# Kernel optimization log

Hardware: AMD Instinct MI355X
Metric: run time of the kernel (lower is better)

The kernel has to match this reference:

```python
import jax, jax.numpy as jnp
import numpy as np

HIDDEN = 768
MLP = 4 * HIDDEN

def layernorm(x, g, b, eps=1e-5):
    mu = jnp.mean(x, axis=-1, keepdims=True)
    var = jnp.var(x, axis=-1, keepdims=True)
    return (x - mu) * jax.lax.rsqrt(var + eps) * g + b

def setup_inputs() -> dict:
    key = jax.random.key(0)
    ks = jax.random.split(key, 10)
    b, l, h = 8, 1024, HIDDEN
    s = 1.0 / np.sqrt(h)
    inp = {
        "x": jax.random.normal(ks[0], (b, l, h), dtype=jnp.float32),
        "Wq": jax.random.normal(ks[1], (h, h), dtype=jnp.float32) * s,
        "Wk": jax.random.normal(ks[2], (h, h), dtype=jnp.float32) * s,
        "Wv": jax.random.normal(ks[3], (h, h), dtype=jnp.float32) * s,
        "Wo": jax.random.normal(ks[4], (h, h), dtype=jnp.float32) * s,
        "W1": jax.random.normal(ks[5], (h, MLP), dtype=jnp.float32) * s,
        "b1": jnp.zeros((MLP,), dtype=jnp.float32),
        "W2": jax.random.normal(ks[6], (MLP, h), dtype=jnp.float32) * (1.0 / np.sqrt(MLP)),
        "b2": jnp.zeros((h,), dtype=jnp.float32),
        "g1": jnp.ones((h,), dtype=jnp.float32),
        "be1": jnp.zeros((h,), dtype=jnp.float32),
        "g2": jnp.ones((h,), dtype=jnp.float32),
        "be2": jnp.zeros((h,), dtype=jnp.float32),
        "n_heads": 12,
    }
    return inp

def reference(x, Wq, Wk, Wv, Wo, W1, b1, W2, b2, g1, be1, g2, be2, n_heads):
    b, l, h = x.shape
    d = h // n_heads
    # NOTE: faithful to source — heads are the LAST axis of a plain reshape,
    # and the second einsum contracts with K (not V), reproducing the original code.
    q = (x @ Wq).reshape(b, l, d, n_heads)
    k = (x @ Wk).reshape(b, l, d, n_heads)
    v = (x @ Wv).reshape(b, l, d, n_heads)  # computed but unused downstream, as in source
    scores = jnp.einsum('bldn,bmdn->blmn', q, k) / (d ** 0.5)
    attn = jax.nn.softmax(scores, axis=2)  # softmax over m (dim=2), as in source
    ctx = jnp.einsum('blmn,bmdn->bldn', attn, k).reshape(b, l, h)
    attn_out = ctx @ Wo
    x = x + attn_out
    x = layernorm(x, g1, be1)
    ff = (jax.nn.gelu(x @ W1 + b1, approximate=False) @ W2) + b2
    x = x + ff
    x = layernorm(x, g2, be2)
    return x
```

## Files before the change

### kernel.cpp

```cpp
#include <hip/hip_runtime.h>
#include <math.h>

typedef unsigned short u16;
typedef unsigned int u32;
typedef short bf16x8 __attribute__((ext_vector_type(8)));
typedef float f32x4 __attribute__((ext_vector_type(4)));

#define MFMA(a, b, c) __builtin_amdgcn_mfma_f32_16x16x32_bf16((a), (b), (c), 0, 0, 0)

#define GLOAD_LDS16(g, l)                                                              \
    __builtin_amdgcn_global_load_lds((const __attribute__((address_space(1))) void*)(g), \
                                     (__attribute__((address_space(3))) void*)(l), 16, 0, 0)

__device__ __forceinline__ u16 f2bf(float f) {
    u32 u = __float_as_uint(f);
    u32 r = (u + 0x7fffu + ((u >> 16) & 1u)) >> 16;
    return (u16)r;
}

__device__ __forceinline__ float fast_gelu(float z) {
    float u = fminf(1.5957691216f * z * (1.0f + 0.044715f * z * z), 80.0f);
    float e = __expf(u);
    float r = __builtin_amdgcn_rcpf(e + 1.0f);
    return z * e * r;
}

__global__ __launch_bounds__(256) void f32_to_bf16_k(const float* __restrict__ in,
                                                     u16* __restrict__ out) {
    size_t i = ((size_t)blockIdx.x * 256 + threadIdx.x) * 8;
    const float4* p = reinterpret_cast<const float4*>(in + i);
    float4 a = p[0], b = p[1];
    union { u16 u[8]; uint4 v; } o;
    o.u[0] = f2bf(a.x); o.u[1] = f2bf(a.y); o.u[2] = f2bf(a.z); o.u[3] = f2bf(a.w);
    o.u[4] = f2bf(b.x); o.u[5] = f2bf(b.y); o.u[6] = f2bf(b.z); o.u[7] = f2bf(b.w);
    *reinterpret_cast<uint4*>(out + i) = o.v;
}

__global__ __launch_bounds__(256) void transpose_bf16_k(const float* __restrict__ in,
                                                        u16* __restrict__ out,
                                                        int K, int N) {
    __shared__ float tile[64][65];
    int k0 = blockIdx.y * 64, n0 = blockIdx.x * 64;
    int t = threadIdx.x;
    for (int p = 0; p < 16; p++) {
        int idx = t + p * 256;
        int r = idx >> 6, c = idx & 63;
        tile[r][c] = in[(size_t)(k0 + r) * N + n0 + c];
    }
    __syncthreads();
    for (int p = 0; p < 16; p++) {
        int idx = t + p * 256;
        int nr = idx >> 6, nc = idx & 63;
        out[(size_t)(n0 + nr) * K + k0 + nc] = f2bf(tile[nc][nr]);
    }
}

__global__ __launch_bounds__(256) void transpose_wo_k(const float* __restrict__ in,
                                                      u16* __restrict__ out) {
    __shared__ float tile[96][65];
    int k0 = blockIdx.y * 96, n0 = blockIdx.x * 64;
    int t = threadIdx.x;
    for (int p = 0; p < 24; p++) {
        int idx = t + p * 256;
        int r = idx >> 6, c = idx & 63;
        tile[r][c] = in[(size_t)(k0 + r) * 768 + n0 + c];
    }
    __syncthreads();
    for (int p = 0; p < 3; p++) {
        int idx = t + p * 256;
        int c = idx / 12, n = idx % 12;
        union { u16 u[8]; uint4 v; } o;
        for (int j = 0; j < 8; j++) o.u[j] = f2bf(tile[j * 12 + n][c]);
        *reinterpret_cast<uint4*>(&out[(size_t)(n0 + c) * 768 + n * 64 + blockIdx.y * 8]) = o.v;
    }
}

__global__ __launch_bounds__(256) void head_pack_k(const u16* __restrict__ in, int ld,
                                                   u16* __restrict__ out) {
    __shared__ u16 tile[16 * 768];
    int b = blockIdx.y;
    int l0 = blockIdx.x * 16;
    int t = threadIdx.x;
    for (int p = 0; p < 6; p++) {
        int c = t + p * 256;
        int li = c / 96, dc = c % 96;
        *reinterpret_cast<uint4*>(&tile[li * 768 + dc * 8]) =
            *reinterpret_cast<const uint4*>(&in[(size_t)(b * 1024 + l0 + li) * ld + dc * 8]);
    }
    __syncthreads();
    for (int p = 0; p < 6; p++) {
        int c = t + p * 256;
        int n = c >> 7, rem = c & 127, li = rem >> 3, k8 = rem & 7;
        union { u16 u[8]; uint4 v; } o;
        for (int j = 0; j < 8; j++) o.u[j] = tile[li * 768 + (k8 * 8 + j) * 12 + n];
        *reinterpret_cast<uint4*>(&out[(size_t)((b * 12 + n) * 1024 + l0 + li) * 64 + k8 * 8]) = o.v;
    }
}

template <int EPI, int TM, bool AH = false>
__global__ __launch_bounds__(256) void gemm_bt_k(const u16* __restrict__ A,
                                                 const u16* __restrict__ BT,
                                                 int M, int N, int K, int NBX,
                                                 float* __restrict__ outF,
                                                 u16* __restrict__ outB,
                                                 const float* __restrict__ resid,
                                                 const float* __restrict__ bias) {
    constexpr int MI = TM / 32;
    constexpr int NS = (TM == 64) ? 4 : 3;
    __shared__ __align__(16) u16 As[NS][TM * 32];
    __shared__ __align__(16) u16 Bs[NS][128 * 32];

    int L = blockIdx.x;
    int bx = (L >> 3) % NBX;
    int by = (L / (8 * NBX)) * 8 + (L & 7);
    int m0 = by * TM, n0 = bx * 128;

    int t = threadIdx.x;
    int wave = t >> 6, lane = t & 63;
    int wr = (wave >> 1) * (TM / 2), wc = (wave & 1) * 64;
    int ln = lane & 15, quad = lane >> 4;
    int sw = quad ^ ((ln >> 1) & 3);

    int e0 = t, e1 = t + 256;
    int r0 = e0 >> 2, c0 = (e0 & 3) ^ ((r0 >> 1) & 3);
    int r1 = e1 >> 2, c1 = (e1 & 3) ^ ((r1 >> 1) & 3);
    const u16* A0 = A + (size_t)(m0 + r0) * K + c0 * 8;
    const u16* A1 = A + (size_t)(m0 + r1) * K + c1 * 8;
    const u16* B0 = BT + (size_t)(n0 + r0) * K + c0 * 8;
    const u16* B1 = BT + (size_t)(n0 + r1) * K + c1 * 8;
    const u16* Abase = nullptr;
    if constexpr (AH) {
        int m = m0 + r0;
        Abase = A + ((size_t)(m >> 10) * 12288 + (m & 1023)) * 64;
    }

    int nk = K >> 5;

    f32x4 acc[MI][4];
    for (int i = 0; i < MI; i++)
        for (int j = 0; j < 4; j++)
            for (int r = 0; r < 4; r++) acc[i][j][r] = 0.0f;

    for (int s = 0; s < NS - 1; s++) {
        if constexpr (AH) {
            int col8 = s * 4 + c0;
            GLOAD_LDS16(Abase + (col8 >> 3) * 65536 + (col8 & 7) * 8, &As[s][e0 * 8]);
        } else {
            GLOAD_LDS16(A0 + s * 32, &As[s][e0 * 8]);
            if constexpr (TM == 128) GLOAD_LDS16(A1 + s * 32, &As[s][e1 * 8]);
        }
        GLOAD_LDS16(B0 + s * 32, &Bs[s][e0 * 8]);
        GLOAD_LDS16(B1 + s * 32, &Bs[s][e1 * 8]);
    }

    for (int k = 0; k < nk; k++) {
        if constexpr (TM == 64) asm volatile("s_waitcnt vmcnt(6)" ::: "memory");
        else                    asm volatile("s_waitcnt vmcnt(4)" ::: "memory");
        asm volatile("s_barrier" ::: "memory");
        {
            int ks = k + NS - 1 < nk ? k + NS - 1 : nk - 1;
            int bi = (k + NS - 1) % NS;
            if constexpr (AH) {
                int col8 = ks * 4 + c0;
                GLOAD_LDS16(Abase + (col8 >> 3) * 65536 + (col8 & 7) * 8, &As[bi][e0 * 8]);
            } else {
                GLOAD_LDS16(A0 + ks * 32, &As[bi][e0 * 8]);
                if constexpr (TM == 128) GLOAD_LDS16(A1 + ks * 32, &As[bi][e1 * 8]);
            }
            GLOAD_LDS16(B0 + ks * 32, &Bs[bi][e0 * 8]);
            GLOAD_LDS16(B1 + ks * 32, &Bs[bi][e1 * 8]);
        }
        const u16* as = As[k % NS];
        const u16* bs = Bs[k % NS];
        bf16x8 afr[MI], bfr[4];
        for (int i = 0; i < MI; i++)
            afr[i] = *reinterpret_cast<const bf16x8*>(&as[(wr + i * 16 + ln) * 32 + sw * 8]);
        for (int j = 0; j < 4; j++)
            bfr[j] = *reinterpret_cast<const bf16x8*>(&bs[(wc + j * 16 + ln) * 32 + sw * 8]);
        for (int i = 0; i < MI; i++)
            for (int j = 0; j < 4; j++)
                acc[i][j] = MFMA(afr[i], bfr[j], acc[i][j]);
    }

    for (int i = 0; i < MI; i++) {
        for (int j = 0; j < 4; j++) {
            int col = n0 + wc + j * 16 + ln;
            for (int r = 0; r < 4; r++) {
                int row = m0 + wr + i * 16 + quad * 4 + r;
                size_t idx = (size_t)row * N + col;
                float v = acc[i][j][r];
                if constexpr (EPI == 0) {
                    outB[idx] = f2bf(v);
                } else if constexpr (EPI == 1) {
                    outF[idx] = resid[idx] + v;
                } else if constexpr (EPI == 2) {
                    outB[idx] = f2bf(fast_gelu(v + bias[col]));
                } else if constexpr (EPI == 3) {
                    outF[idx] = resid[idx] + v + bias[col];
                } else {
                    outB[idx] = f2bf(col < 768 ? v * 0.125f : v);
                }
            }
        }
    }
}

__global__ __launch_bounds__(256) void attention_k(const u16* __restrict__ QB, int ldq,
                                                   const u16* __restrict__ KH,
                                                   u16* __restrict__ CTXH) {
    __shared__ __align__(16) u16 Ks[64 * 72];
    __shared__ __align__(16) u16 KsT[64 * 72];
    __shared__ __align__(16) u16 Pl[4][16 * 64];
    int bh = blockIdx.y;
    int b = bh / 12, n = bh % 12;
    int l0 = blockIdx.x * 64;
    int t = threadIdx.x, wave = t >> 6, lane = t & 63;
    int ln = lane & 15, quad = lane >> 4;
    int lw = l0 + wave * 16;

    bf16x8 a0, a1;
    {
        union { u16 u[8]; bf16x8 v; } q0, q1;
        const u16* qrow = QB + (size_t)(b * 1024 + lw + ln) * ldq + n;
        for (int j = 0; j < 8; j++) {
            q0.u[j] = qrow[(quad * 8 + j) * 12];
            q1.u[j] = qrow[(32 + quad * 8 + j) * 12];
        }
        a0 = q0.v; a1 = q1.v;
    }

    f32x4 o[4];
    for (int dt = 0; dt < 4; dt++)
        for (int r = 0; r < 4; r++) o[dt][r] = 0.0f;
    float lst[4];
    for (int r = 0; r < 4; r++) lst[r] = 0.0f;

    const u16* Kbase = KH + (size_t)bh * 1024 * 64;
    int mi = t & 63, ds = (t >> 6) * 16;
    int psw = (ln >> 2) & 3;

    union { u16 u[8]; uint4 v; } kva, kvb;
    kva.v = *reinterpret_cast<const uint4*>(&Kbase[(size_t)mi * 64 + ds]);
    kvb.v = *reinterpret_cast<const uint4*>(&Kbase[(size_t)mi * 64 + ds + 8]);

    for (int mb = 0; mb < 16; mb++) {
        __syncthreads();
        *reinterpret_cast<uint4*>(&Ks[mi * 72 + ds]) = kva.v;
        *reinterpret_cast<uint4*>(&Ks[mi * 72 + ds + 8]) = kvb.v;
        for (int j = 0; j < 8; j++) KsT[(ds + j) * 72 + mi] = kva.u[j];
        for (int j = 0; j < 8; j++) KsT[(ds + 8 + j) * 72 + mi] = kvb.u[j];
        __syncthreads();

        {
            int mnext = (mb + 1 < 16 ? mb + 1 : 15) * 64;
            kva.v = *reinterpret_cast<const uint4*>(&Kbase[(size_t)(mnext + mi) * 64 + ds]);
            kvb.v = *reinterpret_cast<const uint4*>(&Kbase[(size_t)(mnext + mi) * 64 + ds + 8]);
        }

        f32x4 st[4];
        for (int nt = 0; nt < 4; nt++) {
            bf16x8 bk0 = *reinterpret_cast<bf16x8*>(&Ks[(nt * 16 + ln) * 72 + quad * 8]);
            bf16x8 bk1 = *reinterpret_cast<bf16x8*>(&Ks[(nt * 16 + ln) * 72 + 32 + quad * 8]);
            f32x4 z;
            for (int r = 0; r < 4; r++) z[r] = 0.0f;
            z = MFMA(a0, bk0, z);
            st[nt] = MFMA(a1, bk1, z);
        }

        for (int r = 0; r < 4; r++) {
            int row = quad * 4 + r;
            float psum = 0.0f;
            for (int nt = 0; nt < 4; nt++) {
                float p = __expf(fminf(st[nt][r], 30.0f));
                psum += p;
                Pl[wave][row * 64 + (((nt * 2 + (ln >> 3)) ^ quad) * 8) + (ln & 7)] = f2bf(p);
            }
            lst[r] += psum;
        }

        bf16x8 pf0 = *reinterpret_cast<bf16x8*>(&Pl[wave][ln * 64 + (quad ^ psw) * 8]);
        bf16x8 pf1 = *reinterpret_cast<bf16x8*>(&Pl[wave][ln * 64 + (quad ^ psw) * 8 + 32]);
        for (int dt = 0; dt < 4; dt++) {
            bf16x8 bk0 = *reinterpret_cast<bf16x8*>(&KsT[(dt * 16 + ln) * 72 + quad * 8]);
            bf16x8 bk1 = *reinterpret_cast<bf16x8*>(&KsT[(dt * 16 + ln) * 72 + 32 + quad * 8]);
            o[dt] = MFMA(pf0, bk0, o[dt]);
            o[dt] = MFMA(pf1, bk1, o[dt]);
        }
    }

    for (int r = 0; r < 4; r++)
        for (int off = 1; off < 16; off <<= 1) lst[r] += __shfl_xor(lst[r], off, 64);

    u16* out = CTXH + (size_t)bh * 1024 * 64;
    for (int r = 0; r < 4; r++) {
        float inv = 1.0f / lst[r];
        int row = lw + quad * 4 + r;
        for (int dt = 0; dt < 4; dt++)
            out[(size_t)row * 64 + dt * 16 + ln] = f2bf(o[dt][r] * inv);
    }
}

__global__ __launch_bounds__(256) void layernorm_k(const float* __restrict__ in,
                                                   float* __restrict__ outF,
                                                   u16* __restrict__ outB,
                                                   const float* __restrict__ g,
                                                   const float* __restrict__ be) {
    __shared__ float red[8];
    int row = blockIdx.x;
    int t = threadIdx.x;
    const float* p = in + (size_t)row * 768;
    float v0 = p[t], v1 = p[t + 256], v2 = p[t + 512];
    float s = v0 + v1 + v2;
    float ss = v0 * v0 + v1 * v1 + v2 * v2;
    for (int off = 32; off >= 1; off >>= 1) {
        s += __shfl_xor(s, off, 64);
        ss += __shfl_xor(ss, off, 64);
    }
    int wave = t >> 6, lane = t & 63;
    if (lane == 0) { red[wave] = s; red[4 + wave] = ss; }
    __syncthreads();
    float S = red[0] + red[1] + red[2] + red[3];
    float SS = red[4] + red[5] + red[6] + red[7];
    float mean = S * (1.0f / 768.0f);
    float var = SS * (1.0f / 768.0f) - mean * mean;
    float rstd = rsqrtf(var + 1e-5f);
    float o0 = (v0 - mean) * rstd * g[t] + be[t];
    float o1 = (v1 - mean) * rstd * g[t + 256] + be[t + 256];
    float o2 = (v2 - mean) * rstd * g[t + 512] + be[t + 512];
    float* q = outF + (size_t)row * 768;
    q[t] = o0; q[t + 256] = o1; q[t + 512] = o2;
    if (outB) {
        u16* qb = outB + (size_t)row * 768;
        qb[t] = f2bf(o0); qb[t + 256] = f2bf(o1); qb[t + 512] = f2bf(o2);
    }
}

extern "C" void kernel_launch(void* const* d_in, const int* in_sizes, int n_in,
                              void* d_out, int out_size, void* d_ws, size_t ws_size,
                              hipStream_t stream) {
    const float* x   = (const float*)d_in[0];
    const float* Wq  = (const float*)d_in[1];
    const float* Wk  = (const float*)d_in[2];
    const float* Wo  = (const float*)d_in[4];
    const float* W1  = (const float*)d_in[5];
    const float* b1  = (const float*)d_in[6];
    const float* W2  = (const float*)d_in[7];
    const float* b2  = (const float*)d_in[8];
    const float* g1  = (const float*)d_in[9];
    const float* be1 = (const float*)d_in[10];
    const float* g2  = (const float*)d_in[11];
    const float* be2 = (const float*)d_in[12];
    float* out = (float*)d_out;

    const int S = 8192, H = 768, MLP4 = 3072, H2 = 1536;

    char* ws = (char*)d_ws;
    u16* XB   = (u16*)ws;  ws += (size_t)S * H * 2;
    u16* WQKT = (u16*)ws;  ws += (size_t)H2 * H * 2;
    u16* WOT  = (u16*)ws;  ws += (size_t)H * H * 2;
    u16* W1T  = (u16*)ws;  ws += (size_t)H * MLP4 * 2;
    u16* W2T  = (u16*)ws;  ws += (size_t)H * MLP4 * 2;
    u16* QKB  = (u16*)ws;  ws += (size_t)S * H2 * 2;
    u16* KH   = (u16*)ws;  ws += (size_t)S * H * 2;
    float* Y  = (float*)ws; ws += (size_t)S * H * 4;
    u16* HB   = (u16*)ws;  ws += (size_t)S * MLP4 * 2;

    u16* CTXH = XB;
    u16* X1B  = QKB;

    f32_to_bf16_k<<<(S * H) / 2048, 256, 0, stream>>>(x, XB);
    transpose_bf16_k<<<dim3(12, 12), 256, 0, stream>>>(Wq, WQKT, H, H);
    transpose_bf16_k<<<dim3(12, 12), 256, 0, stream>>>(Wk, WQKT + (size_t)H * H, H, H);
    transpose_wo_k<<<dim3(12, 8), 256, 0, stream>>>(Wo, WOT);
    transpose_bf16_k<<<dim3(48, 12), 256, 0, stream>>>(W1, W1T, H, MLP4);
    transpose_bf16_k<<<dim3(12, 48), 256, 0, stream>>>(W2, W2T, MLP4, H);

    gemm_bt_k<4, 128><<<12 * 64, 256, 0, stream>>>(XB, WQKT, S, H2, H, 12, nullptr, QKB, nullptr, nullptr);

    head_pack_k<<<dim3(64, 8), 256, 0, stream>>>(QKB + H, H2, KH);
    attention_k<<<dim3(16, 96), 256, 0, stream>>>(QKB, H2, KH, CTXH);

    gemm_bt_k<1, 64, true><<<6 * 128, 256, 0, stream>>>(CTXH, WOT, S, H, H, 6, Y, nullptr, x, nullptr);
    layernorm_k<<<S, 256, 0, stream>>>(Y, Y, X1B, g1, be1);

    gemm_bt_k<2, 128><<<24 * 64, 256, 0, stream>>>(X1B, W1T, S, MLP4, H, 24, nullptr, HB, nullptr, b1);
    gemm_bt_k<3, 64><<<6 * 128, 256, 0, stream>>>(HB, W2T, S, H, MLP4, 6, Y, nullptr, Y, b2);
    layernorm_k<<<S, 256, 0, stream>>>(Y, out, nullptr, g2, be2);
}
```

Measured before the change: 412.4 us.

## Merge weight prep into one kernel and use 128x256 tiles for wide GEMMs

Replaces the six separate cast and transpose launches with a single prep kernel that dispatches on block index. Adds a larger-tile GEMM (128x256, 4x8 MFMA fragments per wave, 3-stage pipeline, launch bounds min 2 blocks) for the QK projection and the W1+GELU GEMM, which raises arithmetic intensity per LDS load. The costs are many more accumulator registers per thread and fewer blocks, so occupancy and wave balance may suffer. The smaller GEMMs stay on the 64-row tile kernel.

```diff
diff --git a/kernel.cpp b/kernel.cpp
--- a/kernel.cpp
+++ b/kernel.cpp
@@ -25,9 +25,8 @@
     return z * e * r;
 }
 
-__global__ __launch_bounds__(256) void f32_to_bf16_k(const float* __restrict__ in,
-                                                     u16* __restrict__ out) {
-    size_t i = ((size_t)blockIdx.x * 256 + threadIdx.x) * 8;
+__device__ void dev_xcast(const float* __restrict__ in, u16* __restrict__ out, int blk) {
+    size_t i = ((size_t)blk * 256 + threadIdx.x) * 8;
     const float4* p = reinterpret_cast<const float4*>(in + i);
     float4 a = p[0], b = p[1];
     union { u16 u[8]; uint4 v; } o;
@@ -36,42 +35,67 @@
     *reinterpret_cast<uint4*>(out + i) = o.v;
 }
 
-__global__ __launch_bounds__(256) void transpose_bf16_k(const float* __restrict__ in,
-                                                        u16* __restrict__ out,
-                                                        int K, int N) {
-    __shared__ float tile[64][65];
-    int k0 = blockIdx.y * 64, n0 = blockIdx.x * 64;
+__device__ void dev_transpose(const float* __restrict__ in, u16* __restrict__ out,
+                              int K, int N, int bx, int by, float* tile ) {
+    int k0 = by * 64, n0 = bx * 64;
     int t = threadIdx.x;
     for (int p = 0; p < 16; p++) {
         int idx = t + p * 256;
         int r = idx >> 6, c = idx & 63;
-        tile[r][c] = in[(size_t)(k0 + r) * N + n0 + c];
+        tile[r * 65 + c] = in[(size_t)(k0 + r) * N + n0 + c];
     }
     __syncthreads();
     for (int p = 0; p < 16; p++) {
         int idx = t + p * 256;
         int nr = idx >> 6, nc = idx & 63;
-        out[(size_t)(n0 + nr) * K + k0 + nc] = f2bf(tile[nc][nr]);
-    }
-}
-
-__global__ __launch_bounds__(256) void transpose_wo_k(const float* __restrict__ in,
-                                                      u16* __restrict__ out) {
-    __shared__ float tile[96][65];
-    int k0 = blockIdx.y * 96, n0 = blockIdx.x * 64;
+        out[(size_t)(n0 + nr) * K + k0 + nc] = f2bf(tile[nc * 65 + nr]);
+    }
+}
+
+__device__ void dev_wo(const float* __restrict__ in, u16* __restrict__ out,
+                       int bx, int by, float* tile ) {
+    int k0 = by * 96, n0 = bx * 64;
     int t = threadIdx.x;
     for (int p = 0; p < 24; p++) {
         int idx = t + p * 256;
         int r = idx >> 6, c = idx & 63;
-        tile[r][c] = in[(size_t)(k0 + r) * 768 + n0 + c];
+        tile[r * 65 + c] = in[(size_t)(k0 + r) * 768 + n0 + c];
     }
     __syncthreads();
     for (int p = 0; p < 3; p++) {
         int idx = t + p * 256;
         int c = idx / 12, n = idx % 12;
         union { u16 u[8]; uint4 v; } o;
-        for (int j = 0; j < 8; j++) o.u[j] = f2bf(tile[j * 12 + n][c]);
-        *reinterpret_cast<uint4*>(&out[(size_t)(n0 + c) * 768 + n * 64 + blockIdx.y * 8]) = o.v;
+        for (int j = 0; j < 8; j++) o.u[j] = f2bf(tile[(j * 12 + n) * 65 + c]);
+        *reinterpret_cast<uint4*>(&out[(size_t)(n0 + c) * 768 + n * 64 + by * 8]) = o.v;
+    }
+}
+
+__global__ __launch_bounds__(256) void prep_k(const float* __restrict__ x,
+                                              const float* __restrict__ Wq,
+                                              const float* __restrict__ Wk,
+                                              const float* __restrict__ Wo,
+                                              const float* __restrict__ W1,
+                                              const float* __restrict__ W2,
+                                              u16* __restrict__ XB,
+                                              u16* __restrict__ WQKT,
+                                              u16* __restrict__ WOT,
+                                              u16* __restrict__ W1T,
+                                              u16* __restrict__ W2T) {
+    __shared__ float tile[96 * 65];
+    int bid = blockIdx.x;
+    if (bid < 3072) {
+        dev_xcast(x, XB, bid);
+    } else if (bid < 3216) {
+        int b = bid - 3072; dev_transpose(Wq, WQKT, 768, 768, b % 12, b / 12, tile);
+    } else if (bid < 3360) {
+        int b = bid - 3216; dev_transpose(Wk, WQKT + (size_t)768 * 768, 768, 768, b % 12, b / 12, tile);
+    } else if (bid < 3456) {
+        int b = bid - 3360; dev_wo(Wo, WOT, b % 12, b / 12, tile);
+    } else if (bid < 4032) {
+        int b = bid - 3456; dev_transpose(W1, W1T, 768, 3072, b % 48, b / 48, tile);
+    } else {
+        int b = bid - 4032; dev_transpose(W2, W2T, 3072, 768, b % 12, b / 12, tile);
     }
 }
 
@@ -97,27 +121,107 @@
     }
 }
 
-template <int EPI, int TM, bool AH = false>
+template <int EPI>
+__global__ __launch_bounds__(256, 2) void gemm_big_k(const u16* __restrict__ A,
+                                                     const u16* __restrict__ BT,
+                                                     int M, int N, int K, int NBX,
+                                                     u16* __restrict__ outB,
+                                                     const float* __restrict__ bias) {
+    __shared__ __align__(16) u16 As[3][128 * 32];
+    __shared__ __align__(16) u16 Bs[3][256 * 32];
+    int L = blockIdx.x;
+    int bx = (L >> 3) % NBX;
+    int by = (L / (8 * NBX)) * 8 + (L & 7);
+    int m0 = by * 128, n0 = bx * 256;
+    int t = threadIdx.x, wave = t >> 6, lane = t & 63;
+    int wr = (wave >> 1) * 64, wc = (wave & 1) * 128;
+    int ln = lane & 15, quad = lane >> 4;
+    int sw = quad ^ ((ln >> 1) & 3);
+
+    int ra0 = t >> 2,          ca0 = (t & 3) ^ ((ra0 >> 1) & 3);
+    int ra1 = (t + 256) >> 2,  ca1 = (t & 3) ^ ((ra1 >> 1) & 3);
+    const u16* Ap0 = A + (size_t)(m0 + ra0) * K + ca0 * 8;
+    const u16* Ap1 = A + (size_t)(m0 + ra1) * K + ca1 * 8;
+    const u16* Bp[4];
+    int eoff[4];
+    for (int g = 0; g < 4; g++) {
+        int e = t + 256 * g;
+        int r = e >> 2, c = (e & 3) ^ ((r >> 1) & 3);
+        Bp[g] = BT + (size_t)(n0 + r) * K + c * 8;
+        eoff[g] = e * 8;
+    }
+
+    int nk = K >> 5;
+
+    f32x4 acc[4][8];
+    for (int i = 0; i < 4; i++)
+        for (int j = 0; j < 8; j++)
+            for (int r = 0; r < 4; r++) acc[i][j][r] = 0.0f;
+
+    for (int s = 0; s < 2; s++) {
+        GLOAD_LDS16(Ap0 + s * 32, &As[s][t * 8]);
+        GLOAD_LDS16(Ap1 + s * 32, &As[s][(t + 256) * 8]);
+        for (int g = 0; g < 4; g++) GLOAD_LDS16(Bp[g] + s * 32, &Bs[s][eoff[g]]);
+    }
+
+    for (int k = 0; k < nk; k++) {
+        asm volatile("s_waitcnt vmcnt(6)" ::: "memory");
+        asm volatile("s_barrier" ::: "memory");
+        {
+            int ks = k + 2 < nk ? k + 2 : nk - 1;
+            int bi = (k + 2) % 3;
+            GLOAD_LDS16(Ap0 + ks * 32, &As[bi][t * 8]);
+            GLOAD_LDS16(Ap1 + ks * 32, &As[bi][(t + 256) * 8]);
+            for (int g = 0; g < 4; g++) GLOAD_LDS16(Bp[g] + ks * 32, &Bs[bi][eoff[g]]);
+        }
+        const u16* as = As[k % 3];
+        const u16* bs = Bs[k % 3];
+        bf16x8 afr[4], bfr[8];
+        for (int i = 0; i < 4; i++)
+            afr[i] = *reinterpret_cast<const bf16x8*>(&as[(wr + i * 16 + ln) * 32 + sw * 8]);
+        for (int j = 0; j < 8; j++)
+            bfr[j] = *reinterpret_cast<const bf16x8*>(&bs[(wc + j * 16 + ln) * 32 + sw * 8]);
+        for (int i = 0; i < 4; i++)
+            for (int j = 0; j < 8; j++)
+                acc[i][j] = MFMA(afr[i], bfr[j], acc[i][j]);
+    }
+
+    for (int i = 0; i < 4; i++) {
+        for (int j = 0; j < 8; j++) {
+            int col = n0 + wc + j * 16 + ln;
+            for (int r = 0; r < 4; r++) {
+                int row = m0 + wr + i * 16 + quad * 4 + r;
+                size_t idx = (size_t)row * N + col;
+                float v = acc[i][j][r];
+                if constexpr (EPI == 2) {
+                    outB[idx] = f2bf(fast_gelu(v + bias[col]));
+                } else {
+                    outB[idx] = f2bf(col < 768 ? v * 0.125f : v);
+                }
+            }
+        }
+    }
+}
+
+template <int EPI, bool AH = false>
 __global__ __launch_bounds__(256) void gemm_bt_k(const u16* __restrict__ A,
                                                  const u16* __restrict__ BT,
                                                  int M, int N, int K, int NBX,
                                                  float* __restrict__ outF,
-                                                 u16* __restrict__ outB,
                                                  const float* __restrict__ resid,
                                                  const float* __restrict__ bias) {
-    constexpr int MI = TM / 32;
-    constexpr int NS = (TM == 64) ? 4 : 3;
-    __shared__ __align__(16) u16 As[NS][TM * 32];
+    constexpr int NS = 4;
+    __shared__ __align__(16) u16 As[NS][64 * 32];
     __shared__ __align__(16) u16 Bs[NS][128 * 32];
 
     int L = blockIdx.x;
     int bx = (L >> 3) % NBX;
     int by = (L / (8 * NBX)) * 8 + (L & 7);
-    int m0 = by * TM, n0 = bx * 128;
+    int m0 = by * 64, n0 = bx * 128;
 
     int t = threadIdx.x;
     int wave = t >> 6, lane = t & 63;
-    int wr = (wave >> 1) * (TM / 2), wc = (wave & 1) * 64;
+    int wr = (wave >> 1) * 32, wc = (wave & 1) * 64;
     int ln = lane & 15, quad = lane >> 4;
     int sw = quad ^ ((ln >> 1) & 3);
 
@@ -125,7 +229,6 @@
     int r0 = e0 >> 2, c0 = (e0 & 3) ^ ((r0 >> 1) & 3);
     int r1 = e1 >> 2, c1 = (e1 & 3) ^ ((r1 >> 1) & 3);
     const u16* A0 = A + (size_t)(m0 + r0) * K + c0 * 8;
-    const u16* A1 = A + (size_t)(m0 + r1) * K + c1 * 8;
     const u16* B0 = BT + (size_t)(n0 + r0) * K + c0 * 8;
     const u16* B1 = BT + (size_t)(n0 + r1) * K + c1 * 8;
     const u16* Abase = nullptr;
@@ -136,8 +239,8 @@
 
     int nk = K >> 5;
 
-    f32x4 acc[MI][4];
-    for (int i = 0; i < MI; i++)
+    f32x4 acc[2][4];
+    for (int i = 0; i < 2; i++)
         for (int j = 0; j < 4; j++)
             for (int r = 0; r < 4; r++) acc[i][j][r] = 0.0f;
 
@@ -147,15 +250,13 @@
             GLOAD_LDS16(Abase + (col8 >> 3) * 65536 + (col8 & 7) * 8, &As[s][e0 * 8]);
         } else {
             GLOAD_LDS16(A0 + s * 32, &As[s][e0 * 8]);
-            if constexpr (TM == 128) GLOAD_LDS16(A1 + s * 32, &As[s][e1 * 8]);
         }
         GLOAD_LDS16(B0 + s * 32, &Bs[s][e0 * 8]);
         GLOAD_LDS16(B1 + s * 32, &Bs[s][e1 * 8]);
     }
 
     for (int k = 0; k < nk; k++) {
-        if constexpr (TM == 64) asm volatile("s_waitcnt vmcnt(6)" ::: "memory");
-        else                    asm volatile("s_waitcnt vmcnt(4)" ::: "memory");
+        asm volatile("s_waitcnt vmcnt(6)" ::: "memory");
         asm volatile("s_barrier" ::: "memory");
         {
             int ks = k + NS - 1 < nk ? k + NS - 1 : nk - 1;
@@ -165,40 +266,33 @@
                 GLOAD_LDS16(Abase + (col8 >> 3) * 65536 + (col8 & 7) * 8, &As[bi][e0 * 8]);
             } else {
                 GLOAD_LDS16(A0 + ks * 32, &As[bi][e0 * 8]);
-                if constexpr (TM == 128) GLOAD_LDS16(A1 + ks * 32, &As[bi][e1 * 8]);
             }
             GLOAD_LDS16(B0 + ks * 32, &Bs[bi][e0 * 8]);
             GLOAD_LDS16(B1 + ks * 32, &Bs[bi][e1 * 8]);
         }
         const u16* as = As[k % NS];
         const u16* bs = Bs[k % NS];
-        bf16x8 afr[MI], bfr[4];
-        for (int i = 0; i < MI; i++)
+        bf16x8 afr[2], bfr[4];
+        for (int i = 0; i < 2; i++)
             afr[i] = *reinterpret_cast<const bf16x8*>(&as[(wr + i * 16 + ln) * 32 + sw * 8]);
         for (int j = 0; j < 4; j++)
             bfr[j] = *reinterpret_cast<const bf16x8*>(&bs[(wc + j * 16 + ln) * 32 + sw * 8]);
-        for (int i = 0; i < MI; i++)
+        for (int i = 0; i < 2; i++)
             for (int j = 0; j < 4; j++)
                 acc[i][j] = MFMA(afr[i], bfr[j], acc[i][j]);
     }
 
-    for (int i = 0; i < MI; i++) {
+    for (int i = 0; i < 2; i++) {
         for (int j = 0; j < 4; j++) {
             int col = n0 + wc + j * 16 + ln;
             for (int r = 0; r < 4; r++) {
                 int row = m0 + wr + i * 16 + quad * 4 + r;
                 size_t idx = (size_t)row * N + col;
                 float v = acc[i][j][r];
-                if constexpr (EPI == 0) {
-                    outB[idx] = f2bf(v);
-                } else if constexpr (EPI == 1) {
+                if constexpr (EPI == 1) {
                     outF[idx] = resid[idx] + v;
-                } else if constexpr (EPI == 2) {
-                    outB[idx] = f2bf(fast_gelu(v + bias[col]));
-                } else if constexpr (EPI == 3) {
+                } else {
                     outF[idx] = resid[idx] + v + bias[col];
-                } else {
-                    outB[idx] = f2bf(col < 768 ? v * 0.125f : v);
                 }
             }
         }
@@ -368,22 +462,17 @@
     u16* CTXH = XB;
     u16* X1B  = QKB;
 
-    f32_to_bf16_k<<<(S * H) / 2048, 256, 0, stream>>>(x, XB);
-    transpose_bf16_k<<<dim3(12, 12), 256, 0, stream>>>(Wq, WQKT, H, H);
-    transpose_bf16_k<<<dim3(12, 12), 256, 0, stream>>>(Wk, WQKT + (size_t)H * H, H, H);
-    transpose_wo_k<<<dim3(12, 8), 256, 0, stream>>>(Wo, WOT);
-    transpose_bf16_k<<<dim3(48, 12), 256, 0, stream>>>(W1, W1T, H, MLP4);
-    transpose_bf16_k<<<dim3(12, 48), 256, 0, stream>>>(W2, W2T, MLP4, H);
-
-    gemm_bt_k<4, 128><<<12 * 64, 256, 0, stream>>>(XB, WQKT, S, H2, H, 12, nullptr, QKB, nullptr, nullptr);
+    prep_k<<<4608, 256, 0, stream>>>(x, Wq, Wk, Wo, W1, W2, XB, WQKT, WOT, W1T, W2T);
+
+    gemm_big_k<4><<<384, 256, 0, stream>>>(XB, WQKT, S, H2, H, 6, QKB, nullptr);
 
     head_pack_k<<<dim3(64, 8), 256, 0, stream>>>(QKB + H, H2, KH);
     attention_k<<<dim3(16, 96), 256, 0, stream>>>(QKB, H2, KH, CTXH);
 
-    gemm_bt_k<1, 64, true><<<6 * 128, 256, 0, stream>>>(CTXH, WOT, S, H, H, 6, Y, nullptr, x, nullptr);
+    gemm_bt_k<1, true><<<6 * 128, 256, 0, stream>>>(CTXH, WOT, S, H, H, 6, Y, x, nullptr);
     layernorm_k<<<S, 256, 0, stream>>>(Y, Y, X1B, g1, be1);
 
-    gemm_bt_k<2, 128><<<24 * 64, 256, 0, stream>>>(X1B, W1T, S, MLP4, H, 24, nullptr, HB, nullptr, b1);
-    gemm_bt_k<3, 64><<<6 * 128, 256, 0, stream>>>(HB, W2T, S, H, MLP4, 6, Y, nullptr, Y, b2);
+    gemm_big_k<2><<<768, 256, 0, stream>>>(X1B, W1T, S, MLP4, H, 12, HB, b1);
+    gemm_bt_k<3><<<6 * 128, 256, 0, stream>>>(HB, W2T, S, H, MLP4, 6, Y, Y, b2);
     layernorm_k<<<S, 256, 0, stream>>>(Y, out, nullptr, g2, be2);
 }
```

Measured after the change: 452.2 us. 1.1x slower.

## Merge weight prep into one kernel and scatter QK GEMM output into head-major layout

Applied to the files above, without the earlier changes.

Merges the activation cast and all weight transposes into a single prep kernel dispatched by block index, which removes five kernel launches. The QK projection GEMM epilogue now writes Q and K directly in per-head [b,n,l,d] layout, so the separate head_pack kernel is gone and attention can load Q with vector reads instead of strided gathers. The cost is scattered 2-byte stores in the GEMM epilogue, which may coalesce poorly.

```diff
diff --git a/kernel.cpp b/kernel.cpp
--- a/kernel.cpp
+++ b/kernel.cpp
@@ -25,9 +25,8 @@
     return z * e * r;
 }
 
-__global__ __launch_bounds__(256) void f32_to_bf16_k(const float* __restrict__ in,
-                                                     u16* __restrict__ out) {
-    size_t i = ((size_t)blockIdx.x * 256 + threadIdx.x) * 8;
+__device__ void dev_xcast(const float* __restrict__ in, u16* __restrict__ out, int blk) {
+    size_t i = ((size_t)blk * 256 + threadIdx.x) * 8;
     const float4* p = reinterpret_cast<const float4*>(in + i);
     float4 a = p[0], b = p[1];
     union { u16 u[8]; uint4 v; } o;
@@ -36,64 +35,67 @@
     *reinterpret_cast<uint4*>(out + i) = o.v;
 }
 
-__global__ __launch_bounds__(256) void transpose_bf16_k(const float* __restrict__ in,
-                                                        u16* __restrict__ out,
-                                                        int K, int N) {
-    __shared__ float tile[64][65];
-    int k0 = blockIdx.y * 64, n0 = blockIdx.x * 64;
+__device__ void dev_transpose(const float* __restrict__ in, u16* __restrict__ out,
+                              int K, int N, int bx, int by, float* tile ) {
+    int k0 = by * 64, n0 = bx * 64;
     int t = threadIdx.x;
     for (int p = 0; p < 16; p++) {
         int idx = t + p * 256;
         int r = idx >> 6, c = idx & 63;
-        tile[r][c] = in[(size_t)(k0 + r) * N + n0 + c];
+        tile[r * 65 + c] = in[(size_t)(k0 + r) * N + n0 + c];
     }
     __syncthreads();
     for (int p = 0; p < 16; p++) {
         int idx = t + p * 256;
         int nr = idx >> 6, nc = idx & 63;
-        out[(size_t)(n0 + nr) * K + k0 + nc] = f2bf(tile[nc][nr]);
-    }
-}
-
-__global__ __launch_bounds__(256) void transpose_wo_k(const float* __restrict__ in,
-                                                      u16* __restrict__ out) {
-    __shared__ float tile[96][65];
-    int k0 = blockIdx.y * 96, n0 = blockIdx.x * 64;
+        out[(size_t)(n0 + nr) * K + k0 + nc] = f2bf(tile[nc * 65 + nr]);
+    }
+}
+
+__device__ void dev_wo(const float* __restrict__ in, u16* __restrict__ out,
+                       int bx, int by, float* tile ) {
+    int k0 = by * 96, n0 = bx * 64;
     int t = threadIdx.x;
     for (int p = 0; p < 24; p++) {
         int idx = t + p * 256;
         int r = idx >> 6, c = idx & 63;
-        tile[r][c] = in[(size_t)(k0 + r) * 768 + n0 + c];
+        tile[r * 65 + c] = in[(size_t)(k0 + r) * 768 + n0 + c];
     }
     __syncthreads();
     for (int p = 0; p < 3; p++) {
         int idx = t + p * 256;
         int c = idx / 12, n = idx % 12;
         union { u16 u[8]; uint4 v; } o;
-        for (int j = 0; j < 8; j++) o.u[j] = f2bf(tile[j * 12 + n][c]);
-        *reinterpret_cast<uint4*>(&out[(size_t)(n0 + c) * 768 + n * 64 + blockIdx.y * 8]) = o.v;
-    }
-}
-
-__global__ __launch_bounds__(256) void head_pack_k(const u16* __restrict__ in, int ld,
-                                                   u16* __restrict__ out) {
-    __shared__ u16 tile[16 * 768];
-    int b = blockIdx.y;
-    int l0 = blockIdx.x * 16;
-    int t = threadIdx.x;
-    for (int p = 0; p < 6; p++) {
-        int c = t + p * 256;
-        int li = c / 96, dc = c % 96;
-        *reinterpret_cast<uint4*>(&tile[li * 768 + dc * 8]) =
-            *reinterpret_cast<const uint4*>(&in[(size_t)(b * 1024 + l0 + li) * ld + dc * 8]);
-    }
-    __syncthreads();
-    for (int p = 0; p < 6; p++) {
-        int c = t + p * 256;
-        int n = c >> 7, rem = c & 127, li = rem >> 3, k8 = rem & 7;
-        union { u16 u[8]; uint4 v; } o;
-        for (int j = 0; j < 8; j++) o.u[j] = tile[li * 768 + (k8 * 8 + j) * 12 + n];
-        *reinterpret_cast<uint4*>(&out[(size_t)((b * 12 + n) * 1024 + l0 + li) * 64 + k8 * 8]) = o.v;
+        for (int j = 0; j < 8; j++) o.u[j] = f2bf(tile[(j * 12 + n) * 65 + c]);
+        *reinterpret_cast<uint4*>(&out[(size_t)(n0 + c) * 768 + n * 64 + by * 8]) = o.v;
+    }
+}
+
+__global__ __launch_bounds__(256) void prep_k(const float* __restrict__ x,
+                                              const float* __restrict__ Wq,
+                                              const float* __restrict__ Wk,
+                                              const float* __restrict__ Wo,
+                                              const float* __restrict__ W1,
+                                              const float* __restrict__ W2,
+                                              u16* __restrict__ XB,
+                                              u16* __restrict__ WQKT,
+                                              u16* __restrict__ WOT,
+                                              u16* __restrict__ W1T,
+                                              u16* __restrict__ W2T) {
+    __shared__ float tile[96 * 65];
+    int bid = blockIdx.x;
+    if (bid < 3072) {
+        dev_xcast(x, XB, bid);
+    } else if (bid < 3216) {
+        int b = bid - 3072; dev_transpose(Wq, WQKT, 768, 768, b % 12, b / 12, tile);
+    } else if (bid < 3360) {
+        int b = bid - 3216; dev_transpose(Wk, WQKT + (size_t)768 * 768, 768, 768, b % 12, b / 12, tile);
+    } else if (bid < 3456) {
+        int b = bid - 3360; dev_wo(Wo, WOT, b % 12, b / 12, tile);
+    } else if (bid < 4032) {
+        int b = bid - 3456; dev_transpose(W1, W1T, 768, 3072, b % 48, b / 48, tile);
+    } else {
+        int b = bid - 4032; dev_transpose(W2, W2T, 3072, 768, b % 12, b / 12, tile);
     }
 }
 
@@ -185,49 +187,50 @@
     for (int i = 0; i < MI; i++) {
         for (int j = 0; j < 4; j++) {
             int col = n0 + wc + j * 16 + ln;
-            for (int r = 0; r < 4; r++) {
-                int row = m0 + wr + i * 16 + quad * 4 + r;
-                size_t idx = (size_t)row * N + col;
-                float v = acc[i][j][r];
-                if constexpr (EPI == 0) {
-                    outB[idx] = f2bf(v);
-                } else if constexpr (EPI == 1) {
-                    outF[idx] = resid[idx] + v;
-                } else if constexpr (EPI == 2) {
-                    outB[idx] = f2bf(fast_gelu(v + bias[col]));
-                } else if constexpr (EPI == 3) {
-                    outF[idx] = resid[idx] + v + bias[col];
-                } else {
-                    outB[idx] = f2bf(col < 768 ? v * 0.125f : v);
+            if constexpr (EPI == 4) {
+                bool isQ = col < 768;
+                int cc = isQ ? col : col - 768;
+                int n = cc % 12, d = cc / 12;
+                float scl = isQ ? 0.125f : 1.0f;
+                u16* base = outB + (isQ ? 0 : 6291456) + (size_t)n * 65536 + d;
+                for (int r = 0; r < 4; r++) {
+                    int row = m0 + wr + i * 16 + quad * 4 + r;
+                    base[(size_t)(row >> 10) * 786432 + (size_t)(row & 1023) * 64] =
+                        f2bf(acc[i][j][r] * scl);
+                }
+            } else {
+                for (int r = 0; r < 4; r++) {
+                    int row = m0 + wr + i * 16 + quad * 4 + r;
+                    size_t idx = (size_t)row * N + col;
+                    float v = acc[i][j][r];
+                    if constexpr (EPI == 1) {
+                        outF[idx] = resid[idx] + v;
+                    } else if constexpr (EPI == 2) {
+                        outB[idx] = f2bf(fast_gelu(v + bias[col]));
+                    } else if constexpr (EPI == 3) {
+                        outF[idx] = resid[idx] + v + bias[col];
+                    }
                 }
             }
         }
     }
 }
 
-__global__ __launch_bounds__(256) void attention_k(const u16* __restrict__ QB, int ldq,
+__global__ __launch_bounds__(256) void attention_k(const u16* __restrict__ QH,
                                                    const u16* __restrict__ KH,
                                                    u16* __restrict__ CTXH) {
     __shared__ __align__(16) u16 Ks[64 * 72];
     __shared__ __align__(16) u16 KsT[64 * 72];
     __shared__ __align__(16) u16 Pl[4][16 * 64];
     int bh = blockIdx.y;
-    int b = bh / 12, n = bh % 12;
     int l0 = blockIdx.x * 64;
     int t = threadIdx.x, wave = t >> 6, lane = t & 63;
     int ln = lane & 15, quad = lane >> 4;
     int lw = l0 + wave * 16;
 
-    bf16x8 a0, a1;
-    {
-        union { u16 u[8]; bf16x8 v; } q0, q1;
-        const u16* qrow = QB + (size_t)(b * 1024 + lw + ln) * ldq + n;
-        for (int j = 0; j < 8; j++) {
-            q0.u[j] = qrow[(quad * 8 + j) * 12];
-            q1.u[j] = qrow[(32 + quad * 8 + j) * 12];
-        }
-        a0 = q0.v; a1 = q1.v;
-    }
+    const u16* qrow = QH + (size_t)bh * 65536 + (size_t)(lw + ln) * 64;
+    bf16x8 a0 = *reinterpret_cast<const bf16x8*>(qrow + quad * 8);
+    bf16x8 a1 = *reinterpret_cast<const bf16x8*>(qrow + 32 + quad * 8);
 
     f32x4 o[4];
     for (int dt = 0; dt < 4; dt++)
@@ -235,7 +238,7 @@
     float lst[4];
     for (int r = 0; r < 4; r++) lst[r] = 0.0f;
 
-    const u16* Kbase = KH + (size_t)bh * 1024 * 64;
+    const u16* Kbase = KH + (size_t)bh * 65536;
     int mi = t & 63, ds = (t >> 6) * 16;
     int psw = (ln >> 2) & 3;
 
@@ -291,7 +294,7 @@
     for (int r = 0; r < 4; r++)
         for (int off = 1; off < 16; off <<= 1) lst[r] += __shfl_xor(lst[r], off, 64);
 
-    u16* out = CTXH + (size_t)bh * 1024 * 64;
+    u16* out = CTXH + (size_t)bh * 65536;
     for (int r = 0; r < 4; r++) {
         float inv = 1.0f / lst[r];
         int row = lw + quad * 4 + r;
@@ -360,25 +363,18 @@
     u16* WOT  = (u16*)ws;  ws += (size_t)H * H * 2;
     u16* W1T  = (u16*)ws;  ws += (size_t)H * MLP4 * 2;
     u16* W2T  = (u16*)ws;  ws += (size_t)H * MLP4 * 2;
-    u16* QKB  = (u16*)ws;  ws += (size_t)S * H2 * 2;
-    u16* KH   = (u16*)ws;  ws += (size_t)S * H * 2;
+    u16* QKH  = (u16*)ws;  ws += (size_t)S * H2 * 2;
     float* Y  = (float*)ws; ws += (size_t)S * H * 4;
     u16* HB   = (u16*)ws;  ws += (size_t)S * MLP4 * 2;
 
     u16* CTXH = XB;
-    u16* X1B  = QKB;
-
-    f32_to_bf16_k<<<(S * H) / 2048, 256, 0, stream>>>(x, XB);
-    transpose_bf16_k<<<dim3(12, 12), 256, 0, stream>>>(Wq, WQKT, H, H);
-    transpose_bf16_k<<<dim3(12, 12), 256, 0, stream>>>(Wk, WQKT + (size_t)H * H, H, H);
-    transpose_wo_k<<<dim3(12, 8), 256, 0, stream>>>(Wo, WOT);
-    transpose_bf16_k<<<dim3(48, 12), 256, 0, stream>>>(W1, W1T, H, MLP4);
-    transpose_bf16_k<<<dim3(12, 48), 256, 0, stream>>>(W2, W2T, MLP4, H);
-
-    gemm_bt_k<4, 128><<<12 * 64, 256, 0, stream>>>(XB, WQKT, S, H2, H, 12, nullptr, QKB, nullptr, nullptr);
-
-    head_pack_k<<<dim3(64, 8), 256, 0, stream>>>(QKB + H, H2, KH);
-    attention_k<<<dim3(16, 96), 256, 0, stream>>>(QKB, H2, KH, CTXH);
+    u16* X1B  = QKH;
+
+    prep_k<<<4608, 256, 0, stream>>>(x, Wq, Wk, Wo, W1, W2, XB, WQKT, WOT, W1T, W2T);
+
+    gemm_bt_k<4, 128><<<12 * 64, 256, 0, stream>>>(XB, WQKT, S, H2, H, 12, nullptr, QKH, nullptr, nullptr);
+
+    attention_k<<<dim3(16, 96), 256, 0, stream>>>(QKH, QKH + (size_t)S * H, CTXH);
 
     gemm_bt_k<1, 64, true><<<6 * 128, 256, 0, stream>>>(CTXH, WOT, S, H, H, 6, Y, nullptr, x, nullptr);
     layernorm_k<<<S, 256, 0, stream>>>(Y, Y, X1B, g1, be1);
```

Result: slower. 424.7 us (+3.0%).
